# Kernel optimization log

Measured on AMD Instinct MI355X. Metric: run time of the kernel, lower is better.

Reference implementation:

```python
import jax, jax.numpy as jnp
import numpy as np

V, E = 1024, 2048
IN_DIM = OUT_DIM = 256
H = 4
D = OUT_DIM // H           # head_dim = 64
ENC = 8                    # causal_encoding_dim
HID = 32                   # causal_gate_hidden
LN_EPS = 1e-5


def setup_inputs() -> dict:
    key = jax.random.key(0)
    ks = jax.random.split(key, 12)
    s = 0.05
    return {
        "h": jax.random.normal(ks[0], (V, IN_DIM), jnp.float32),
        "causal_effects": jax.random.normal(ks[1], (V, V, 2), jnp.float32),
        "W": jax.random.normal(ks[2], (IN_DIM, OUT_DIM), jnp.float32) * s,
        "attn_w": jax.random.normal(ks[3], (2 * D + ENC,), jnp.float32) * s,
        "enc_w": jax.random.normal(ks[4], (2, ENC), jnp.float32) * s,
        "enc_b": jnp.zeros((ENC,), jnp.float32),
        "g1_w": jax.random.normal(ks[5], (2, HID), jnp.float32) * s,
        "g1_b": jnp.zeros((HID,), jnp.float32),
        "g2_w": jax.random.normal(ks[6], (HID, 1), jnp.float32) * s,
        "g2_b": jnp.zeros((1,), jnp.float32),
        "ln_g": jnp.ones((OUT_DIM,), jnp.float32),
        "ln_b": jnp.zeros((OUT_DIM,), jnp.float32),
        "incidence": jax.random.randint(ks[7], (V, E), 0, 2, dtype=jnp.int32),
    }


def _chan_forward(h, causal_effects, W, attn_w, enc_w, enc_b,
                  g1_w, g1_b, g2_w, g2_b, ln_g, ln_b, incidence):
    num_v, num_e = incidence.shape
    M = (incidence > 0).astype(h.dtype)                 # [V,E] binary membership
    mask = incidence > 0                                 # [V,E] bool

    Wh = h @ W                                           # [V,O]
    Whh = Wh.reshape(num_v, H, D)                        # [V,H,D]

    cnt_e = M.sum(axis=0)                                # [E] edge sizes
    deg_e = jnp.maximum(cnt_e, 1.0)
    h_bar = (M.T @ Wh) / deg_e[:, None]                  # [E,O] edge means
    hbh = h_bar.reshape(num_e, H, D)                     # [E,H,D]

    # number of "other" members for each (v,e): |e| - [v in e]
    n_ve = cnt_e[None, :] - M                            # [V,E]
    inv_n = jnp.where(n_ve > 0, 1.0 / jnp.maximum(n_ve, 1.0), 0.0)

    # per-(v,e) mean causal effect over other members of e
    diag_ce = jnp.diagonal(causal_effects, axis1=0, axis2=1).T   # [V,2]
    S = jnp.einsum('vuk,ue->vek', causal_effects, M)             # sum over members
    S = S - M[:, :, None] * diag_ce[:, None, :]                  # exclude u==v
    ce_mean = S * inv_n[:, :, None]                              # [V,E,2] (0 if no others)

    c = ce_mean @ enc_w + enc_b                                  # [V,E,ENC]

    a_v, a_e, a_c = attn_w[:D], attn_w[D:2 * D], attn_w[2 * D:]
    scores = (jnp.einsum('vhd,d->vh', Whh, a_v)[:, None, :]
              + jnp.einsum('ehd,d->eh', hbh, a_e)[None, :, :]
              + (c @ a_c)[:, :, None])                           # [V,E,H]
    scores = jax.nn.leaky_relu(scores, 0.2)
    neg = jnp.asarray(-1e9, scores.dtype)
    scores = jnp.where(mask[:, :, None], scores, neg)
    alpha = jax.nn.softmax(scores, axis=1) * mask[:, :, None].astype(scores.dtype)
    ap = alpha * inv_n[:, :, None]                               # alpha / n_others

    # causal gate psi(v,u) in [0,1], per vertex pair
    z = jax.nn.relu(causal_effects @ g1_w + g1_b)                # [V,V,HID]
    G = jax.nn.sigmoid((z @ g2_w)[..., 0] + g2_b[0])             # [V,V]

    # spread attention over edge members: A[v,u,h] = sum_e ap[v,e,h] * M[u,e]
    A = jnp.einsum('veh,ue->vuh', ap, M)                         # [V,V,H]
    out = jnp.einsum('vuh,vu,uhd->vhd', A, G, Whh)               # gated messages
    # remove self-contribution (u == v)
    s_v = ap.sum(axis=1)                                         # [V,H]
    Gvv = jnp.diagonal(G)                                        # [V]
    out = out - s_v[:, :, None] * Gvv[:, None, None] * Whh       # [V,H,D]

    out = out.reshape(num_v, -1) + Wh                            # residual (in==out dim)
    mu = out.mean(axis=-1, keepdims=True)
    var = out.var(axis=-1, keepdims=True)
    out = (out - mu) / jnp.sqrt(var + LN_EPS) * ln_g + ln_b
    return out                                                   # dropout = identity (eval)


def reference(h, causal_effects, W, attn_w, enc_w, enc_b,
              g1_w, g1_b, g2_w, g2_b, ln_g, ln_b, incidence):
    return _chan_forward(h, causal_effects, W, attn_w, enc_w, enc_b,
                         g1_w, g1_b, g2_w, g2_b, ln_g, ln_b, incidence)
```

## Files before the change

### kernel.cpp

```cpp
#include <hip/hip_runtime.h>
#include <hip/hip_bf16.h>

#define NV 1024
#define NE 2048

typedef unsigned short u16;
typedef __attribute__((ext_vector_type(8))) short bf16x8;
typedef __attribute__((ext_vector_type(4))) float f32x4;
typedef __attribute__((ext_vector_type(16))) float f32x16;

__device__ __forceinline__ float bf2f(u16 u) { return __uint_as_float(((unsigned)u) << 16); }
__device__ __forceinline__ u16 f2bf(float f) {
  unsigned x = __float_as_uint(f);
  return (u16)((x + 0x7fffu + ((x >> 16) & 1u)) >> 16);
}

#define GLL(src, dst)                                                        \
  __builtin_amdgcn_global_load_lds(                                          \
      (const __attribute__((address_space(1))) void*)(src),                  \
      (__attribute__((address_space(3))) void*)(dst), 16, 0, 0)

template <int N>
__device__ __forceinline__ void waitcnt_vm() {
  if constexpr (N == 0) asm volatile("s_waitcnt vmcnt(0)" ::: "memory");
  else if constexpr (N == 3) asm volatile("s_waitcnt vmcnt(3)" ::: "memory");
  else if constexpr (N == 8) asm volatile("s_waitcnt vmcnt(8)" ::: "memory");
}
__device__ __forceinline__ void waitcnt_lgkm0() {
  asm volatile("s_waitcnt lgkmcnt(0)" ::: "memory");
}
__device__ __forceinline__ void barrier_raw() { __builtin_amdgcn_s_barrier(); }

__device__ __forceinline__ void invswz(int g, int& row, int& kq) {
  int pb = g * 16;
  int lb = pb ^ ((((pb >> 8) & 1) << 6) | (((pb >> 7) & 1) << 5) |
                 ((((pb >> 6) ^ (pb >> 8)) & 1) << 4));
  row = lb >> 6;
  kq = lb & 63;
}
__device__ __forceinline__ int fwdswz(int la) { return la ^ (((la >> 6) & 7) << 4); }

template <int EPI>
__global__ __launch_bounds__(128) void mfma_w2(
    const u16* __restrict__ A, int lda, long sA,
    const u16* __restrict__ BT, int ldb, long sBT,
    void* __restrict__ Cp, int ldc, long sC, int K,
    const float* __restrict__ Gm) {
  __shared__ __align__(16) char L[32768];
  const int t = threadIdx.x;
  const int wave = t >> 6, lane = t & 63;
  const int l31 = lane & 31, lh = lane >> 5;
  const int m0 = blockIdx.x * 64, n0 = blockIdx.y * 64;
  const int zz = blockIdx.z;
  const char* Ab = (const char*)(A + sA * zz);
  const char* Bb = (const char*)(BT + sBT * zz);
  const long lda2 = (long)lda * 2, ldb2 = (long)ldb * 2;

  char* Lw = L + wave * 16384;
  char* A0 = Lw;
  char* B0 = Lw + 4096;
  char* A1 = Lw + 8192;
  char* B1 = Lw + 12288;

  int rL[4], qL[4];
#pragma unroll
  for (int j = 0; j < 4; j++) invswz(j * 64 + lane, rL[j], qL[j]);

  f32x16 acc[2][2] = {};

  auto stage = [&](char* Ad, char* Bd, int tile) {
    waitcnt_lgkm0();
    const long kb = (long)tile * 64;
#pragma unroll
    for (int j = 0; j < 4; j++)
      GLL(Ab + (long)(m0 + rL[j]) * lda2 + kb + qL[j], Ad + j * 1024);
#pragma unroll
    for (int j = 0; j < 4; j++)
      GLL(Bb + (long)(n0 + rL[j]) * ldb2 + kb + qL[j], Bd + j * 1024);
  };
  auto comp = [&](const char* A_, const char* B_) {
#pragma unroll
    for (int kss = 0; kss < 2; kss++) {
      bf16x8 af[2], bfv[2];
#pragma unroll
      for (int mi = 0; mi < 2; mi++)
        af[mi] = *(const bf16x8*)(A_ + fwdswz((mi * 32 + l31) * 64 + kss * 32 + lh * 16));
#pragma unroll
      for (int ni = 0; ni < 2; ni++)
        bfv[ni] = *(const bf16x8*)(B_ + fwdswz((ni * 32 + l31) * 64 + kss * 32 + lh * 16));
#pragma unroll
      for (int mi = 0; mi < 2; mi++)
#pragma unroll
        for (int ni = 0; ni < 2; ni++)
          acc[mi][ni] =
              __builtin_amdgcn_mfma_f32_32x32x16_bf16(af[mi], bfv[ni], acc[mi][ni], 0, 0, 0);
    }
  };

  const int nt2 = K / 64;
  const int tb = wave * nt2;
  stage(A0, B0, tb);
  for (int i = 0; i + 2 < nt2; i += 2) {
    stage(A1, B1, tb + i + 1);
    waitcnt_vm<8>();
    comp(A0, B0);
    stage(A0, B0, tb + i + 2);
    waitcnt_vm<8>();
    comp(A1, B1);
  }
  stage(A1, B1, tb + nt2 - 1);
  waitcnt_vm<8>();
  comp(A0, B0);
  waitcnt_vm<0>();
  comp(A1, B1);

  waitcnt_lgkm0();
  float4* myD = (float4*)Lw;
  const float* otD = (const float*)(L + (wave ^ 1) * 16384);
  if (wave == 0) {
#pragma unroll
    for (int ni = 0; ni < 2; ni++)
#pragma unroll
      for (int r4 = 0; r4 < 4; r4++)
        myD[r4 * 128 + ni * 64 + lane] =
            make_float4(acc[1][ni][r4 * 4 + 0], acc[1][ni][r4 * 4 + 1],
                        acc[1][ni][r4 * 4 + 2], acc[1][ni][r4 * 4 + 3]);
  } else {
#pragma unroll
    for (int ni = 0; ni < 2; ni++)
#pragma unroll
      for (int r4 = 0; r4 < 4; r4++)
        myD[r4 * 128 + ni * 64 + lane] =
            make_float4(acc[0][ni][r4 * 4 + 0], acc[0][ni][r4 * 4 + 1],
                        acc[0][ni][r4 * 4 + 2], acc[0][ni][r4 * 4 + 3]);
  }
  __syncthreads();

  auto store_one = [&](int m, int n, float vv) {
    if constexpr (EPI == 0) {
      ((float*)Cp)[sC * zz + (long)m * ldc + n] = vv;
    } else {
      ((u16*)Cp)[sC * zz + (long)m * ldc + n] = f2bf(vv * Gm[(long)m * NV + n]);
    }
  };
  if (wave == 0) {
#pragma unroll
    for (int ni = 0; ni < 2; ni++)
#pragma unroll
      for (int r = 0; r < 16; r++) {
        float vv = acc[0][ni][r] + otD[((r >> 2) * 128 + ni * 64 + lane) * 4 + (r & 3)];
        int m = m0 + (r & 3) + 8 * (r >> 2) + 4 * lh;
        store_one(m, n0 + ni * 32 + l31, vv);
      }
  } else {
#pragma unroll
    for (int ni = 0; ni < 2; ni++)
#pragma unroll
      for (int r = 0; r < 16; r++) {
        float vv = acc[1][ni][r] + otD[((r >> 2) * 128 + ni * 64 + lane) * 4 + (r & 3)];
        int m = m0 + 32 + (r & 3) + 8 * (r >> 2) + 4 * lh;
        store_one(m, n0 + ni * 32 + l31, vv);
      }
  }
}

__global__ __launch_bounds__(256) void mfma_bt8(
    const u16* __restrict__ A, const u16* __restrict__ BT,
    float* __restrict__ Cp) {
  constexpr int BM = 128, BN = 64, FM = 4, FN = 2;
  __shared__ __align__(16) char As0[BM * 64];
  __shared__ __align__(16) char As1[BM * 64];
  __shared__ __align__(16) char Bs0[BN * 64];
  __shared__ __align__(16) char Bs1[BN * 64];
  const int t = threadIdx.x;
  const int wave = t >> 6, lane = t & 63;
  const int lhi = lane >> 4, llo = lane & 15;
  const int wm = (wave >> 1) * 64, wn = (wave & 1) * 32;
  const int m0 = blockIdx.y * BM;
  const int zz = blockIdx.z >> 3, ks = blockIdx.z & 7;
  const char* Ab = (const char*)(A + (long)NV * NV * zz + ks * 128);
  const char* Bb = (const char*)(BT + (long)64 * NV * zz + ks * 128);
  const long lda2 = (long)NV * 2, ldb2 = (long)NV * 2;

  int rA0, qA0, rA1, qA1;
  invswz(t, rA0, qA0);
  invswz(t + 256, rA1, qA1);
  const int wofs = (t & 192) * 16;

  f32x4 acc[FM][FN] = {};

  auto stage = [&](char* Ad, char* Bd, int k0) {
    const long kb = (long)k0 * 2;
    GLL(Ab + (long)(m0 + rA0) * lda2 + kb + qA0, Ad + wofs);
    GLL(Ab + (long)(m0 + rA1) * lda2 + kb + qA1, Ad + 4096 + wofs);
    GLL(Bb + (long)rA0 * ldb2 + kb + qA0, Bd + wofs);
  };
  auto compute = [&](const char* A_, const char* B_) {
    bf16x8 af[FM], bfv[FN];
#pragma unroll
    for (int mi = 0; mi < FM; mi++)
      af[mi] = *(const bf16x8*)(A_ + fwdswz((wm + mi * 16 + llo) * 64 + lhi * 16));
#pragma unroll
    for (int ni = 0; ni < FN; ni++)
      bfv[ni] = *(const bf16x8*)(B_ + fwdswz((wn + ni * 16 + llo) * 64 + lhi * 16));
#pragma unroll
    for (int mi = 0; mi < FM; mi++)
#pragma unroll
      for (int ni = 0; ni < FN; ni++)
        acc[mi][ni] =
            __builtin_amdgcn_mfma_f32_16x16x32_bf16(af[mi], bfv[ni], acc[mi][ni], 0, 0, 0);
  };

  stage(As0, Bs0, 0);
  stage(As1, Bs1, 32);
  waitcnt_vm<3>();
  barrier_raw();
  compute(As0, Bs0);
  barrier_raw();
  stage(As0, Bs0, 64);
  waitcnt_vm<3>();
  barrier_raw();
  compute(As1, Bs1);
  barrier_raw();
  stage(As1, Bs1, 96);
  waitcnt_vm<3>();
  barrier_raw();
  compute(As0, Bs0);
  waitcnt_vm<0>();
  barrier_raw();
  compute(As1, Bs1);

#pragma unroll
  for (int mi = 0; mi < FM; mi++)
#pragma unroll
    for (int ni = 0; ni < FN; ni++)
#pragma unroll
      for (int r = 0; r < 4; r++) {
        int m = m0 + wm + mi * 16 + lhi * 4 + r;
        int n = wn + ni * 16 + llo;
        Cp[(long)ks * (NV * 256) + (long)m * 256 + zz * 64 + n] = acc[mi][ni][r];
      }
}

__global__ __launch_bounds__(256) void mm_f32(
    const float* __restrict__ Ap, const float* __restrict__ Bp,
    float* __restrict__ Cp) {
  __shared__ float As[16][68];
  __shared__ float Bs[16][68];
  const int t = threadIdx.x;
  const int tx = t & 15, ty = t >> 4;
  const int m0 = blockIdx.y * 64, n0 = blockIdx.x * 64;
  const int lr = t >> 2, lc4 = (t & 3) * 4;
  const int bk = t >> 4, bn = (t & 15) * 4;
  float acc[4][4] = {};
  for (int k0 = 0; k0 < 256; k0 += 16) {
    float4 a4 = *(const float4*)(Ap + (long)(m0 + lr) * 256 + k0 + lc4);
    As[lc4 + 0][lr] = a4.x;
    As[lc4 + 1][lr] = a4.y;
    As[lc4 + 2][lr] = a4.z;
    As[lc4 + 3][lr] = a4.w;
    float4 b4 = *(const float4*)(Bp + (long)(k0 + bk) * 256 + n0 + bn);
    Bs[bk][bn + 0] = b4.x;
    Bs[bk][bn + 1] = b4.y;
    Bs[bk][bn + 2] = b4.z;
    Bs[bk][bn + 3] = b4.w;
    __syncthreads();
#pragma unroll
    for (int kk = 0; kk < 16; kk++) {
      float a[4], b[4];
      *(float4*)a = *(const float4*)&As[kk][ty * 4];
      *(float4*)b = *(const float4*)&Bs[kk][tx * 4];
#pragma unroll
      for (int i = 0; i < 4; i++)
#pragma unroll
        for (int j = 0; j < 4; j++) acc[i][j] = fmaf(a[i], b[j], acc[i][j]);
    }
    __syncthreads();
  }
#pragma unroll
  for (int i = 0; i < 4; i++)
#pragma unroll
    for (int j = 0; j < 4; j++)
      Cp[(long)(m0 + ty * 4 + i) * 256 + n0 + tx * 4 + j] = acc[i][j];
}

__global__ __launch_bounds__(256) void k_conv(const int* __restrict__ inc,
                                              const float* __restrict__ qe,
                                              u16* __restrict__ Mbf,
                                              u16* __restrict__ Mtbf,
                                              float* __restrict__ part) {
  __shared__ u16 tile[64][65];
  const int e0 = blockIdx.x * 64, v0 = blockIdx.y * 64;
  const int t = threadIdx.x;
#pragma unroll
  for (int p = 0; p < 4; p++) {
    int r = p * 16 + (t >> 4);
    int c4 = (t & 15) * 4;
    int4 q = *(const int4*)(inc + (long)(v0 + r) * NE + e0 + c4);
    ushort4 w;
    w.x = q.x > 0 ? 0x3F80 : 0;
    w.y = q.y > 0 ? 0x3F80 : 0;
    w.z = q.z > 0 ? 0x3F80 : 0;
    w.w = q.w > 0 ? 0x3F80 : 0;
    *(ushort4*)&Mbf[(long)(v0 + r) * NE + e0 + c4] = w;
    tile[c4 + 0][r] = w.x;
    tile[c4 + 1][r] = w.y;
    tile[c4 + 2][r] = w.z;
    tile[c4 + 3][r] = w.w;
  }
  __syncthreads();
#pragma unroll
  for (int p = 0; p < 4; p++) {
    int er = p * 16 + (t >> 4);
    int vc4 = (t & 15) * 4;
    ushort4 w;
    w.x = tile[er][vc4 + 0];
    w.y = tile[er][vc4 + 1];
    w.z = tile[er][vc4 + 2];
    w.w = tile[er][vc4 + 3];
    *(ushort4*)&Mtbf[(long)(e0 + er) * NV + v0 + vc4] = w;
  }
  int er = t >> 2, q4 = t & 3;
  float c = 0, s0 = 0, s1 = 0, s2 = 0, s3 = 0;
  for (int vl = q4 * 16; vl < q4 * 16 + 16; vl++) {
    if (tile[er][vl]) {
      c += 1.f;
      const float* q4p = &qe[(long)(v0 + vl) * 4];
      s0 += q4p[0];
      s1 += q4p[1];
      s2 += q4p[2];
      s3 += q4p[3];
    }
  }
#pragma unroll
  for (int m = 1; m <= 2; m <<= 1) {
    c += __shfl_xor(c, m);
    s0 += __shfl_xor(s0, m);
    s1 += __shfl_xor(s1, m);
    s2 += __shfl_xor(s2, m);
    s3 += __shfl_xor(s3, m);
  }
  if (q4 == 0) {
    int b = blockIdx.y;
    int e = e0 + er;
    part[(0 * 16 + b) * NE + e] = c;
    part[(1 * 16 + b) * NE + e] = s0;
    part[(2 * 16 + b) * NE + e] = s1;
    part[(3 * 16 + b) * NE + e] = s2;
    part[(4 * 16 + b) * NE + e] = s3;
  }
}

__global__ __launch_bounds__(256) void k_trw(const float* __restrict__ Wh,
                                             u16* __restrict__ Whht) {
  __shared__ u16 tile[64][65];
  const int c0 = blockIdx.x * 64, v0 = blockIdx.y * 64;
  const int t = threadIdx.x;
#pragma unroll
  for (int p = 0; p < 4; p++) {
    int r = p * 16 + (t >> 4);
    int c4 = (t & 15) * 4;
    float4 q = *(const float4*)(Wh + (long)(v0 + r) * 256 + c0 + c4);
    tile[c4 + 0][r] = f2bf(q.x);
    tile[c4 + 1][r] = f2bf(q.y);
    tile[c4 + 2][r] = f2bf(q.z);
    tile[c4 + 3][r] = f2bf(q.w);
  }
  __syncthreads();
#pragma unroll
  for (int p = 0; p < 4; p++) {
    int cr = p * 16 + (t >> 4);
    int vc4 = (t & 15) * 4;
    ushort4 w;
    w.x = tile[cr][vc4 + 0];
    w.y = tile[cr][vc4 + 1];
    w.z = tile[cr][vc4 + 2];
    w.w = tile[cr][vc4 + 3];
    *(ushort4*)&Whht[(long)(c0 + cr) * NV + v0 + vc4] = w;
  }
}

__global__ __launch_bounds__(256) void k_qse1(const float* __restrict__ Wh,
                                              const float* __restrict__ attn_w,
                                              float* __restrict__ qv, float* __restrict__ qe) {
  int v = blockIdx.x, t = threadIdx.x;
  int d = t & 63, h = t >> 6;
  float x = Wh[(long)v * 256 + t];
  float pv = x * attn_w[d];
  float pe = x * attn_w[64 + d];
  for (int s = 32; s; s >>= 1) {
    pv += __shfl_down(pv, s);
    pe += __shfl_down(pe, s);
  }
  if (d == 0) {
    qv[v * 4 + h] = pv;
    qe[v * 4 + h] = pe;
  }
}

__global__ __launch_bounds__(256) void k_sered(const float* __restrict__ part,
                                               float* __restrict__ cnt, float* __restrict__ se) {
  int e = blockIdx.x * 256 + threadIdx.x;
  int j = blockIdx.y;
  float s = 0;
  for (int b = 0; b < 16; b++) s += part[(j * 16 + b) * NE + e];
  if (j == 0)
    cnt[e] = s;
  else
    se[e * 4 + (j - 1)] = s;
}

__global__ __launch_bounds__(256) void k_G(const float* __restrict__ ce,
                                           const float* __restrict__ enc_w,
                                           const float* __restrict__ attn_w,
                                           const float* __restrict__ g1w,
                                           const float* __restrict__ g1b,
                                           const float* __restrict__ g2w,
                                           const float* __restrict__ g2b,
                                           float* __restrict__ G, u16* __restrict__ wce) {
  long idx = (long)blockIdx.x * 256 + threadIdx.x;
  float2 c = *(const float2*)(ce + idx * 2);
  float ew0 = 0, ew1 = 0;
#pragma unroll
  for (int j = 0; j < 8; j++) {
    float ac = attn_w[128 + j];
    ew0 += enc_w[j] * ac;
    ew1 += enc_w[8 + j] * ac;
  }
  wce[idx] = f2bf(c.x * ew0 + c.y * ew1);
  float s = g2b[0];
#pragma unroll
  for (int j = 0; j < 32; j++) {
    float zz = fmaxf(c.x * g1w[j] + c.y * g1w[32 + j] + g1b[j], 0.f);
    s = fmaf(zz, g2w[j], s);
  }
  G[idx] = 1.f / (1.f + expf(-s));
}

__global__ __launch_bounds__(256) void k_softmax(
    const float* __restrict__ P, const int* __restrict__ inc, const float* __restrict__ cnt,
    const float* __restrict__ qv, const float* __restrict__ se, const float* __restrict__ ce,
    const float* __restrict__ enc_w, const float* __restrict__ attn_w,
    const float* __restrict__ enc_b, u16* __restrict__ ap, float* __restrict__ sv) {
  int v = blockIdx.x, t = threadIdx.x;
  float ew0 = 0, ew1 = 0, ebac = 0;
#pragma unroll
  for (int j = 0; j < 8; j++) {
    float ac = attn_w[128 + j];
    ew0 += enc_w[j] * ac;
    ew1 += enc_w[8 + j] * ac;
    ebac += enc_b[j] * ac;
  }
  float dce = ce[((long)v * NV + v) * 2] * ew0 + ce[((long)v * NV + v) * 2 + 1] * ew1;
  float svh[4];
#pragma unroll
  for (int hh = 0; hh < 4; hh++) svh[hh] = qv[v * 4 + hh];

  float sc[8][4];
  float invn[8], msk[8];
  float mx[4] = {-3e38f, -3e38f, -3e38f, -3e38f};
  for (int i = 0; i < 8; i++) {
    int e = t + i * 256;
    float cnte = cnt[e];
    float mask = inc[(long)v * NE + e] > 0 ? 1.f : 0.f;
    float nve = cnte - mask;
    float inv = nve > 0.f ? 1.f / nve : 0.f;
    float rdg = 1.f / fmaxf(cnte, 1.f);
    invn[i] = inv;
    msk[i] = mask;
    float cc = inv * (P[(long)v * NE + e] - mask * dce) + ebac;
#pragma unroll
    for (int hh = 0; hh < 4; hh++) {
      float s = svh[hh] + se[e * 4 + hh] * rdg + cc;
      s = s > 0.f ? s : 0.2f * s;
      s = mask > 0.f ? s : -1e9f;
      sc[i][hh] = s;
      mx[hh] = fmaxf(mx[hh], s);
    }
  }
  __shared__ float red[4][256];
#pragma unroll
  for (int hh = 0; hh < 4; hh++) red[hh][t] = mx[hh];
  __syncthreads();
  for (int s = 128; s; s >>= 1) {
    if (t < s)
#pragma unroll
      for (int hh = 0; hh < 4; hh++) red[hh][t] = fmaxf(red[hh][t], red[hh][t + s]);
    __syncthreads();
  }
  float gm[4];
#pragma unroll
  for (int hh = 0; hh < 4; hh++) gm[hh] = red[hh][0];
  __syncthreads();

  float lsum[4] = {0, 0, 0, 0};
  for (int i = 0; i < 8; i++)
#pragma unroll
    for (int hh = 0; hh < 4; hh++) {
      float p = expf(sc[i][hh] - gm[hh]);
      sc[i][hh] = p;
      lsum[hh] += p;
    }
#pragma unroll
  for (int hh = 0; hh < 4; hh++) red[hh][t] = lsum[hh];
  __syncthreads();
  for (int s = 128; s; s >>= 1) {
    if (t < s)
#pragma unroll
      for (int hh = 0; hh < 4; hh++) red[hh][t] += red[hh][t + s];
    __syncthreads();
  }
  float inv_s[4];
#pragma unroll
  for (int hh = 0; hh < 4; hh++) inv_s[hh] = 1.f / red[hh][0];
  __syncthreads();

  float lsv[4] = {0, 0, 0, 0};
  for (int i = 0; i < 8; i++) {
    int e = t + i * 256;
#pragma unroll
    for (int hh = 0; hh < 4; hh++) {
      float a = sc[i][hh] * inv_s[hh] * msk[i] * invn[i];
      ap[(long)hh * NV * NE + (long)v * NE + e] = f2bf(a);
      lsv[hh] += a;
    }
  }
#pragma unroll
  for (int hh = 0; hh < 4; hh++) red[hh][t] = lsv[hh];
  __syncthreads();
  for (int s = 128; s; s >>= 1) {
    if (t < s)
#pragma unroll
      for (int hh = 0; hh < 4; hh++) red[hh][t] += red[hh][t + s];
    __syncthreads();
  }
  if (t == 0)
#pragma unroll
    for (int hh = 0; hh < 4; hh++) sv[v * 4 + hh] = red[hh][0];
}

__global__ __launch_bounds__(256) void k_redln(
    const float* __restrict__ part, const float* __restrict__ Wh,
    const float* __restrict__ G, const float* __restrict__ sv,
    const float* __restrict__ lng, const float* __restrict__ lnb,
    float* __restrict__ out) {
  int v = blockIdx.x, t = threadIdx.x;
  float x = 0.f;
#pragma unroll
  for (int s = 0; s < 8; s++) x += part[(long)s * NV * 256 + (long)v * 256 + t];
  int z = t >> 6;
  float corr = 1.f - sv[v * 4 + z] * G[(long)v * NV + v];
  x += Wh[(long)v * 256 + t] * corr;
  __shared__ float red[256];
  red[t] = x;
  __syncthreads();
  for (int s = 128; s; s >>= 1) {
    if (t < s) red[t] += red[t + s];
    __syncthreads();
  }
  float mu = red[0] * (1.f / 256.f);
  __syncthreads();
  float d = x - mu;
  red[t] = d * d;
  __syncthreads();
  for (int s = 128; s; s >>= 1) {
    if (t < s) red[t] += red[t + s];
    __syncthreads();
  }
  float var = red[0] * (1.f / 256.f);
  out[(long)v * 256 + t] = d / sqrtf(var + 1e-5f) * lng[t] + lnb[t];
}

extern "C" void kernel_launch(void* const* d_in, const int* in_sizes, int n_in,
                              void* d_out, int out_size, void* d_ws, size_t ws_size,
                              hipStream_t stream) {
  const float* h = (const float*)d_in[0];
  const float* ce = (const float*)d_in[1];
  const float* W = (const float*)d_in[2];
  const float* attn_w = (const float*)d_in[3];
  const float* enc_w = (const float*)d_in[4];
  const float* enc_b = (const float*)d_in[5];
  const float* g1w = (const float*)d_in[6];
  const float* g1b = (const float*)d_in[7];
  const float* g2w = (const float*)d_in[8];
  const float* g2b = (const float*)d_in[9];
  const float* lng = (const float*)d_in[10];
  const float* lnb = (const float*)d_in[11];
  const int* inc = (const int*)d_in[12];
  float* out = (float*)d_out;

  size_t off = 0;
  char* base = (char*)d_ws;
  auto alloc = [&](size_t bytes) {
    void* p = base + off;
    off += (bytes + 255) & ~(size_t)255;
    return p;
  };
  float* Wh = (float*)alloc((size_t)NV * 256 * 4);
  float* cnt = (float*)alloc((size_t)NE * 4);
  float* qv = (float*)alloc((size_t)NV * 4 * 4);
  float* qe = (float*)alloc((size_t)NV * 4 * 4);
  float* se = (float*)alloc((size_t)NE * 4 * 4);
  float* sv = (float*)alloc((size_t)NV * 4 * 4);
  float* G = (float*)alloc((size_t)NV * NV * 4);
  u16* wce = (u16*)alloc((size_t)NV * NV * 2);
  u16* Mbf = (u16*)alloc((size_t)NV * NE * 2);
  u16* Whht = (u16*)alloc((size_t)256 * NV * 2);
  float* P = (float*)alloc((size_t)NV * NE * 4);
  u16* ap = (u16*)alloc((size_t)4 * NV * NE * 2);
  u16* Bh = (u16*)alloc((size_t)4 * NV * NV * 2);
  float* part = P;
  u16* Mtbf = Bh;
  float* part8 = P;
  (void)ws_size;
  (void)in_sizes;
  (void)n_in;
  (void)out_size;

  mm_f32<<<dim3(256 / 64, NV / 64), 256, 0, stream>>>(h, W, Wh);
  k_trw<<<dim3(256 / 64, NV / 64), 256, 0, stream>>>(Wh, Whht);
  k_qse1<<<NV, 256, 0, stream>>>(Wh, attn_w, qv, qe);
  k_conv<<<dim3(NE / 64, NV / 64), 256, 0, stream>>>(inc, qe, Mbf, Mtbf, part);
  k_sered<<<dim3(NE / 256, 5), 256, 0, stream>>>(part, cnt, se);
  k_G<<<(NV * NV) / 256, 256, 0, stream>>>(ce, enc_w, attn_w, g1w, g1b, g2w, g2b, G, wce);
  mfma_w2<0><<<dim3(NV / 64, NE / 64, 1), 128, 0, stream>>>(
      wce, NV, 0, Mtbf, NV, 0, P, NE, 0, NV, nullptr);
  k_softmax<<<NV, 256, 0, stream>>>(P, inc, cnt, qv, se, ce, enc_w, attn_w, enc_b, ap, sv);
  mfma_w2<1><<<dim3(NV / 64, NV / 64, 4), 128, 0, stream>>>(
      ap, NE, (long)NV * NE, Mbf, NE, 0, Bh, NV, (long)NV * NV, NE, G);
  mfma_bt8<<<dim3(1, NV / 128, 32), 256, 0, stream>>>(Bh, Whht, part8);
  k_redln<<<NV, 256, 0, stream>>>(part8, Wh, G, sv, lng, lnb, out);
}
```

Measured before the change: 115.3 us.

## Use 128x128 triple-buffered MFMA kernel for gated attention-spread GEMM

Adds a new bf16 MFMA GEMM kernel with 128x128 output tiles, four waves each computing 64x64, and a three-stage global_load_lds pipeline. It replaces the 64x64 two-wave kernel for the batched A = ap·M^T product with the G-gating epilogue. Larger tiles raise data reuse and cut global traffic per FLOP, and the deeper prefetch hides load latency. The cost is fewer blocks (256 instead of 1024) and 48KB of LDS per block, which may lower occupancy. The epilogue still writes scalar bf16 values one at a time.

```diff
diff --git a/kernel.cpp b/kernel.cpp
--- a/kernel.cpp
+++ b/kernel.cpp
@@ -24,6 +24,7 @@
 __device__ __forceinline__ void waitcnt_vm() {
   if constexpr (N == 0) asm volatile("s_waitcnt vmcnt(0)" ::: "memory");
   else if constexpr (N == 3) asm volatile("s_waitcnt vmcnt(3)" ::: "memory");
+  else if constexpr (N == 4) asm volatile("s_waitcnt vmcnt(4)" ::: "memory");
   else if constexpr (N == 8) asm volatile("s_waitcnt vmcnt(8)" ::: "memory");
 }
 __device__ __forceinline__ void waitcnt_lgkm0() {
@@ -39,6 +40,101 @@
   kq = lb & 63;
 }
 __device__ __forceinline__ int fwdswz(int la) { return la ^ (((la >> 6) & 7) << 4); }
+
+template <int EPI>
+__global__ __launch_bounds__(256) void mfma_t128(
+    const u16* __restrict__ A, int lda, long sA,
+    const u16* __restrict__ BT, int ldb, long sBT,
+    void* __restrict__ Cp, int ldc, long sC, int K,
+    const float* __restrict__ Gm) {
+  __shared__ __align__(16) char AB0[16384];
+  __shared__ __align__(16) char AB1[16384];
+  __shared__ __align__(16) char AB2[16384];
+  const int t = threadIdx.x;
+  const int wave = t >> 6, lane = t & 63;
+  const int l31 = lane & 31, lh = lane >> 5;
+  const int wm = (wave >> 1) * 64, wn = (wave & 1) * 64;
+  const int m0 = blockIdx.x * 128, n0 = blockIdx.y * 128;
+  const int zz = blockIdx.z;
+  const char* Ab = (const char*)(A + sA * zz);
+  const char* Bb = (const char*)(BT + sBT * zz);
+  const long lda2 = (long)lda * 2, ldb2 = (long)ldb * 2;
+
+  int rA0, qA0, rA1, qA1;
+  invswz(t, rA0, qA0);
+  invswz(t + 256, rA1, qA1);
+  const int wofs = (t & 192) * 16;
+
+  f32x16 acc[2][2] = {};
+
+  auto stage = [&](char* D, int tile) {
+    const long kb = (long)tile * 64;
+    GLL(Ab + (long)(m0 + rA0) * lda2 + kb + qA0, D + wofs);
+    GLL(Ab + (long)(m0 + rA1) * lda2 + kb + qA1, D + 4096 + wofs);
+    GLL(Bb + (long)(n0 + rA0) * ldb2 + kb + qA0, D + 8192 + wofs);
+    GLL(Bb + (long)(n0 + rA1) * ldb2 + kb + qA1, D + 12288 + wofs);
+  };
+  auto comp = [&](const char* D) {
+    const char* A_ = D;
+    const char* B_ = D + 8192;
+#pragma unroll
+    for (int kss = 0; kss < 2; kss++) {
+      bf16x8 af[2], bfv[2];
+#pragma unroll
+      for (int mi = 0; mi < 2; mi++)
+        af[mi] = *(const bf16x8*)(A_ + fwdswz((wm + mi * 32 + l31) * 64 + kss * 32 + lh * 16));
+#pragma unroll
+      for (int ni = 0; ni < 2; ni++)
+        bfv[ni] = *(const bf16x8*)(B_ + fwdswz((wn + ni * 32 + l31) * 64 + kss * 32 + lh * 16));
+#pragma unroll
+      for (int mi = 0; mi < 2; mi++)
+#pragma unroll
+        for (int ni = 0; ni < 2; ni++)
+          acc[mi][ni] =
+              __builtin_amdgcn_mfma_f32_32x32x16_bf16(af[mi], bfv[ni], acc[mi][ni], 0, 0, 0);
+    }
+  };
+
+  const int nt = K / 32;
+  char* p0 = AB0;
+  char* p1 = AB1;
+  char* p2 = AB2;
+  stage(p0, 0);
+  stage(p1, 1);
+  for (int i = 0; i < nt - 2; i++) {
+    stage(p2, i + 2);
+    waitcnt_vm<8>();
+    barrier_raw();
+    comp(p0);
+    barrier_raw();
+    char* tmp = p0;
+    p0 = p1;
+    p1 = p2;
+    p2 = tmp;
+  }
+  waitcnt_vm<4>();
+  barrier_raw();
+  comp(p0);
+  waitcnt_vm<0>();
+  barrier_raw();
+  comp(p1);
+
+#pragma unroll
+  for (int mi = 0; mi < 2; mi++)
+#pragma unroll
+    for (int ni = 0; ni < 2; ni++)
+#pragma unroll
+      for (int r = 0; r < 16; r++) {
+        int m = m0 + wm + mi * 32 + (r & 3) + 8 * (r >> 2) + 4 * lh;
+        int n = n0 + wn + ni * 32 + l31;
+        float vv = acc[mi][ni][r];
+        if constexpr (EPI == 0) {
+          ((float*)Cp)[sC * zz + (long)m * ldc + n] = vv;
+        } else {
+          ((u16*)Cp)[sC * zz + (long)m * ldc + n] = f2bf(vv * Gm[(long)m * NV + n]);
+        }
+      }
+}
 
 template <int EPI>
 __global__ __launch_bounds__(128) void mfma_w2(
@@ -626,7 +722,7 @@
   mfma_w2<0><<<dim3(NV / 64, NE / 64, 1), 128, 0, stream>>>(
       wce, NV, 0, Mtbf, NV, 0, P, NE, 0, NV, nullptr);
   k_softmax<<<NV, 256, 0, stream>>>(P, inc, cnt, qv, se, ce, enc_w, attn_w, enc_b, ap, sv);
-  mfma_w2<1><<<dim3(NV / 64, NV / 64, 4), 128, 0, stream>>>(
+  mfma_t128<1><<<dim3(NV / 128, NV / 128, 4), 256, 0, stream>>>(
       ap, NE, (long)NV * NE, Mbf, NE, 0, Bh, NV, (long)NV * NV, NE, G);
   mfma_bt8<<<dim3(1, NV / 128, 32), 256, 0, stream>>>(Bh, Whht, part8);
   k_redln<<<NV, 256, 0, stream>>>(part8, Wh, G, sv, lng, lnb, out);
```

Result: slower. 118.3 us (+2.5%).

## Switch two membership GEMMs from bf16 to scaled fp8 MFMA

Applied to the files above, without the earlier changes.

Converts the membership matrices, the weighted causal-effect matrix and the attention probabilities to fp8 (e4m3) with power-of-two prescaling, and runs the two large GEMMs with fp8 MFMA instructions, undoing the scale in the epilogue. This halves the bytes staged through LDS and global memory for those operands and doubles the K covered per tile. The membership matrix stays exact in fp8, but the causal-effect weights and attention probabilities lose precision, which risks accuracy tolerance failures.

```diff
diff --git a/kernel.cpp b/kernel.cpp
--- a/kernel.cpp
+++ b/kernel.cpp
@@ -5,14 +5,33 @@
 #define NE 2048
 
 typedef unsigned short u16;
+typedef unsigned char u8;
 typedef __attribute__((ext_vector_type(8))) short bf16x8;
 typedef __attribute__((ext_vector_type(4))) float f32x4;
 typedef __attribute__((ext_vector_type(16))) float f32x16;
+typedef __attribute__((ext_vector_type(2))) long i64x2;
 
 __device__ __forceinline__ float bf2f(u16 u) { return __uint_as_float(((unsigned)u) << 16); }
 __device__ __forceinline__ u16 f2bf(float f) {
   unsigned x = __float_as_uint(f);
   return (u16)((x + 0x7fffu + ((x >> 16) & 1u)) >> 16);
+}
+__device__ __forceinline__ u8 f2fp8(float f) {
+  unsigned x = __float_as_uint(f);
+  unsigned sgn = (x >> 24) & 0x80;
+  float af = __uint_as_float(x & 0x7fffffff);
+  unsigned q;
+  if (af >= 448.f) {
+    q = 0x7e;
+  } else if (af < 0.015625f) {
+    q = (unsigned)rintf(af * 512.f);
+  } else {
+    unsigned xa = x & 0x7fffffff;
+    xa += 0x7ffff + ((xa >> 20) & 1);
+    q = (xa >> 20) - 960;
+    if (q > 0x7e) q = 0x7e;
+  }
+  return (u8)(sgn | q);
 }
 
 #define GLL(src, dst)                                                        \
@@ -41,10 +60,10 @@
 __device__ __forceinline__ int fwdswz(int la) { return la ^ (((la >> 6) & 7) << 4); }
 
 template <int EPI>
-__global__ __launch_bounds__(128) void mfma_w2(
-    const u16* __restrict__ A, int lda, long sA,
-    const u16* __restrict__ BT, int ldb, long sBT,
-    void* __restrict__ Cp, int ldc, long sC, int K,
+__global__ __launch_bounds__(128) void mfma8_w2(
+    const u8* __restrict__ A, int lda, long sA,
+    const u8* __restrict__ BT, int ldb, long sBT,
+    void* __restrict__ Cp, int ldc, long sC, int K, float unsc,
     const float* __restrict__ Gm) {
   __shared__ __align__(16) char L[32768];
   const int t = threadIdx.x;
@@ -52,9 +71,8 @@
   const int l31 = lane & 31, lh = lane >> 5;
   const int m0 = blockIdx.x * 64, n0 = blockIdx.y * 64;
   const int zz = blockIdx.z;
-  const char* Ab = (const char*)(A + sA * zz);
-  const char* Bb = (const char*)(BT + sBT * zz);
-  const long lda2 = (long)lda * 2, ldb2 = (long)ldb * 2;
+  const u8* Ab = A + sA * zz;
+  const u8* Bb = BT + sBT * zz;
 
   char* Lw = L + wave * 16384;
   char* A0 = Lw;
@@ -73,31 +91,34 @@
     const long kb = (long)tile * 64;
 #pragma unroll
     for (int j = 0; j < 4; j++)
-      GLL(Ab + (long)(m0 + rL[j]) * lda2 + kb + qL[j], Ad + j * 1024);
+      GLL(Ab + (long)(m0 + rL[j]) * lda + kb + qL[j], Ad + j * 1024);
 #pragma unroll
     for (int j = 0; j < 4; j++)
-      GLL(Bb + (long)(n0 + rL[j]) * ldb2 + kb + qL[j], Bd + j * 1024);
+      GLL(Bb + (long)(n0 + rL[j]) * ldb + kb + qL[j], Bd + j * 1024);
   };
   auto comp = [&](const char* A_, const char* B_) {
 #pragma unroll
-    for (int kss = 0; kss < 2; kss++) {
-      bf16x8 af[2], bfv[2];
+    for (int kss2 = 0; kss2 < 2; kss2++) {
+      i64x2 av[2], bv[2];
 #pragma unroll
       for (int mi = 0; mi < 2; mi++)
-        af[mi] = *(const bf16x8*)(A_ + fwdswz((mi * 32 + l31) * 64 + kss * 32 + lh * 16));
+        av[mi] = *(const i64x2*)(A_ + fwdswz((mi * 32 + l31) * 64 + kss2 * 32 + lh * 16));
 #pragma unroll
       for (int ni = 0; ni < 2; ni++)
-        bfv[ni] = *(const bf16x8*)(B_ + fwdswz((ni * 32 + l31) * 64 + kss * 32 + lh * 16));
+        bv[ni] = *(const i64x2*)(B_ + fwdswz((ni * 32 + l31) * 64 + kss2 * 32 + lh * 16));
 #pragma unroll
       for (int mi = 0; mi < 2; mi++)
 #pragma unroll
-        for (int ni = 0; ni < 2; ni++)
-          acc[mi][ni] =
-              __builtin_amdgcn_mfma_f32_32x32x16_bf16(af[mi], bfv[ni], acc[mi][ni], 0, 0, 0);
+        for (int ni = 0; ni < 2; ni++) {
+          acc[mi][ni] = __builtin_amdgcn_mfma_f32_32x32x16_fp8_fp8(
+              av[mi][0], bv[ni][0], acc[mi][ni], 0, 0, 0);
+          acc[mi][ni] = __builtin_amdgcn_mfma_f32_32x32x16_fp8_fp8(
+              av[mi][1], bv[ni][1], acc[mi][ni], 0, 0, 0);
+        }
     }
   };
 
-  const int nt2 = K / 64;
+  const int nt2 = K / 128;
   const int tb = wave * nt2;
   stage(A0, B0, tb);
   for (int i = 0; i + 2 < nt2; i += 2) {
@@ -138,9 +159,9 @@
 
   auto store_one = [&](int m, int n, float vv) {
     if constexpr (EPI == 0) {
-      ((float*)Cp)[sC * zz + (long)m * ldc + n] = vv;
+      ((float*)Cp)[sC * zz + (long)m * ldc + n] = vv * unsc;
     } else {
-      ((u16*)Cp)[sC * zz + (long)m * ldc + n] = f2bf(vv * Gm[(long)m * NV + n]);
+      ((u16*)Cp)[sC * zz + (long)m * ldc + n] = f2bf(vv * unsc * Gm[(long)m * NV + n]);
     }
   };
   if (wave == 0) {
@@ -167,16 +188,16 @@
 __global__ __launch_bounds__(256) void mfma_bt8(
     const u16* __restrict__ A, const u16* __restrict__ BT,
     float* __restrict__ Cp) {
-  constexpr int BM = 128, BN = 64, FM = 4, FN = 2;
-  __shared__ __align__(16) char As0[BM * 64];
-  __shared__ __align__(16) char As1[BM * 64];
-  __shared__ __align__(16) char Bs0[BN * 64];
-  __shared__ __align__(16) char Bs1[BN * 64];
+  constexpr int FM = 4, FN = 2;
+  __shared__ __align__(16) char As0[8192];
+  __shared__ __align__(16) char As1[8192];
+  __shared__ __align__(16) char Bs0[4096];
+  __shared__ __align__(16) char Bs1[4096];
   const int t = threadIdx.x;
   const int wave = t >> 6, lane = t & 63;
   const int lhi = lane >> 4, llo = lane & 15;
   const int wm = (wave >> 1) * 64, wn = (wave & 1) * 32;
-  const int m0 = blockIdx.y * BM;
+  const int m0 = blockIdx.y * 128;
   const int zz = blockIdx.z >> 3, ks = blockIdx.z & 7;
   const char* Ab = (const char*)(A + (long)NV * NV * zz + ks * 128);
   const char* Bb = (const char*)(BT + (long)64 * NV * zz + ks * 128);
@@ -286,10 +307,10 @@
 
 __global__ __launch_bounds__(256) void k_conv(const int* __restrict__ inc,
                                               const float* __restrict__ qe,
-                                              u16* __restrict__ Mbf,
-                                              u16* __restrict__ Mtbf,
+                                              u8* __restrict__ Mbf,
+                                              u8* __restrict__ Mtbf,
                                               float* __restrict__ part) {
-  __shared__ u16 tile[64][65];
+  __shared__ u8 tile[64][68];
   const int e0 = blockIdx.x * 64, v0 = blockIdx.y * 64;
   const int t = threadIdx.x;
 #pragma unroll
@@ -297,12 +318,12 @@
     int r = p * 16 + (t >> 4);
     int c4 = (t & 15) * 4;
     int4 q = *(const int4*)(inc + (long)(v0 + r) * NE + e0 + c4);
-    ushort4 w;
-    w.x = q.x > 0 ? 0x3F80 : 0;
-    w.y = q.y > 0 ? 0x3F80 : 0;
-    w.z = q.z > 0 ? 0x3F80 : 0;
-    w.w = q.w > 0 ? 0x3F80 : 0;
-    *(ushort4*)&Mbf[(long)(v0 + r) * NE + e0 + c4] = w;
+    uchar4 w;
+    w.x = q.x > 0 ? 0x38 : 0;
+    w.y = q.y > 0 ? 0x38 : 0;
+    w.z = q.z > 0 ? 0x38 : 0;
+    w.w = q.w > 0 ? 0x38 : 0;
+    *(uchar4*)&Mbf[(long)(v0 + r) * NE + e0 + c4] = w;
     tile[c4 + 0][r] = w.x;
     tile[c4 + 1][r] = w.y;
     tile[c4 + 2][r] = w.z;
@@ -313,12 +334,12 @@
   for (int p = 0; p < 4; p++) {
     int er = p * 16 + (t >> 4);
     int vc4 = (t & 15) * 4;
-    ushort4 w;
+    uchar4 w;
     w.x = tile[er][vc4 + 0];
     w.y = tile[er][vc4 + 1];
     w.z = tile[er][vc4 + 2];
     w.w = tile[er][vc4 + 3];
-    *(ushort4*)&Mtbf[(long)(e0 + er) * NV + v0 + vc4] = w;
+    *(uchar4*)&Mtbf[(long)(e0 + er) * NV + v0 + vc4] = w;
   }
   int er = t >> 2, q4 = t & 3;
   float c = 0, s0 = 0, s1 = 0, s2 = 0, s3 = 0;
@@ -417,7 +438,7 @@
                                            const float* __restrict__ g1b,
                                            const float* __restrict__ g2w,
                                            const float* __restrict__ g2b,
-                                           float* __restrict__ G, u16* __restrict__ wce) {
+                                           float* __restrict__ G, u8* __restrict__ wce) {
   long idx = (long)blockIdx.x * 256 + threadIdx.x;
   float2 c = *(const float2*)(ce + idx * 2);
   float ew0 = 0, ew1 = 0;
@@ -427,7 +448,7 @@
     ew0 += enc_w[j] * ac;
     ew1 += enc_w[8 + j] * ac;
   }
-  wce[idx] = f2bf(c.x * ew0 + c.y * ew1);
+  wce[idx] = f2fp8((c.x * ew0 + c.y * ew1) * 512.f);
   float s = g2b[0];
 #pragma unroll
   for (int j = 0; j < 32; j++) {
@@ -441,7 +462,7 @@
     const float* __restrict__ P, const int* __restrict__ inc, const float* __restrict__ cnt,
     const float* __restrict__ qv, const float* __restrict__ se, const float* __restrict__ ce,
     const float* __restrict__ enc_w, const float* __restrict__ attn_w,
-    const float* __restrict__ enc_b, u16* __restrict__ ap, float* __restrict__ sv) {
+    const float* __restrict__ enc_b, u8* __restrict__ ap, float* __restrict__ sv) {
   int v = blockIdx.x, t = threadIdx.x;
   float ew0 = 0, ew1 = 0, ebac = 0;
 #pragma unroll
@@ -521,7 +542,7 @@
 #pragma unroll
     for (int hh = 0; hh < 4; hh++) {
       float a = sc[i][hh] * inv_s[hh] * msk[i] * invn[i];
-      ap[(long)hh * NV * NE + (long)v * NE + e] = f2bf(a);
+      ap[(long)hh * NV * NE + (long)v * NE + e] = f2fp8(a * 131072.f);
       lsv[hh] += a;
     }
   }
@@ -603,14 +624,14 @@
   float* se = (float*)alloc((size_t)NE * 4 * 4);
   float* sv = (float*)alloc((size_t)NV * 4 * 4);
   float* G = (float*)alloc((size_t)NV * NV * 4);
-  u16* wce = (u16*)alloc((size_t)NV * NV * 2);
-  u16* Mbf = (u16*)alloc((size_t)NV * NE * 2);
+  u8* wce = (u8*)alloc((size_t)NV * NV);
+  u8* Mbf = (u8*)alloc((size_t)NV * NE);
   u16* Whht = (u16*)alloc((size_t)256 * NV * 2);
   float* P = (float*)alloc((size_t)NV * NE * 4);
-  u16* ap = (u16*)alloc((size_t)4 * NV * NE * 2);
+  u8* ap = (u8*)alloc((size_t)4 * NV * NE);
   u16* Bh = (u16*)alloc((size_t)4 * NV * NV * 2);
   float* part = P;
-  u16* Mtbf = Bh;
+  u8* Mtbf = (u8*)Bh;
   float* part8 = P;
   (void)ws_size;
   (void)in_sizes;
@@ -623,11 +644,11 @@
   k_conv<<<dim3(NE / 64, NV / 64), 256, 0, stream>>>(inc, qe, Mbf, Mtbf, part);
   k_sered<<<dim3(NE / 256, 5), 256, 0, stream>>>(part, cnt, se);
   k_G<<<(NV * NV) / 256, 256, 0, stream>>>(ce, enc_w, attn_w, g1w, g1b, g2w, g2b, G, wce);
-  mfma_w2<0><<<dim3(NV / 64, NE / 64, 1), 128, 0, stream>>>(
-      wce, NV, 0, Mtbf, NV, 0, P, NE, 0, NV, nullptr);
+  mfma8_w2<0><<<dim3(NV / 64, NE / 64, 1), 128, 0, stream>>>(
+      wce, NV, 0, Mtbf, NV, 0, P, NE, 0, NV, 1.f / 512.f, nullptr);
   k_softmax<<<NV, 256, 0, stream>>>(P, inc, cnt, qv, se, ce, enc_w, attn_w, enc_b, ap, sv);
-  mfma_w2<1><<<dim3(NV / 64, NV / 64, 4), 128, 0, stream>>>(
-      ap, NE, (long)NV * NE, Mbf, NE, 0, Bh, NV, (long)NV * NV, NE, G);
+  mfma8_w2<1><<<dim3(NV / 64, NV / 64, 4), 128, 0, stream>>>(
+      ap, NE, (long)NV * NE, Mbf, NE, 0, Bh, NV, (long)NV * NV, NE, 1.f / 131072.f, G);
   mfma_bt8<<<dim3(1, NV / 128, 32), 256, 0, stream>>>(Bh, Whht, part8);
   k_redln<<<NV, 256, 0, stream>>>(part8, Wh, G, sv, lng, lnb, out);
 }
```

After: 99.35 us. 13.8% less time.
